# Kernel tuning notes

Measured on AMD Instinct MI355X. Metric: run time of the kernel, lower is better.

The kernel has to match this reference:

```python
import jax, jax.numpy as jnp
import numpy as np

DIM = 1024


def setup_inputs() -> dict:
    key = jax.random.key(0)
    ks = jax.random.split(key, 10)
    d = DIM
    return {
        "x": jax.random.normal(ks[0], (8, 4096, d), dtype=jnp.float32),
        "A": jax.random.normal(ks[1], (d, d), dtype=jnp.float32) * 0.1,
        "B": jax.random.normal(ks[2], (d, d), dtype=jnp.float32) * 0.1,
        "W_in": jax.random.normal(ks[3], (d, d), dtype=jnp.float32) * (1.0 / np.sqrt(d)),
        "b_in": jax.random.normal(ks[4], (d,), dtype=jnp.float32) * 0.01,
        "W_gate": jax.random.normal(ks[5], (d, d), dtype=jnp.float32) * (1.0 / np.sqrt(d)),
        "b_gate": jax.random.normal(ks[6], (d,), dtype=jnp.float32) * 0.01,
        "W_out": jax.random.normal(ks[7], (d, d), dtype=jnp.float32) * (1.0 / np.sqrt(d)),
        "b_out": jax.random.normal(ks[8], (d,), dtype=jnp.float32) * 0.01,
    }


def reference(x, A, B, W_in, b_in, W_gate, b_gate, W_out, b_out):
    # x: (batch, seq, dim)
    batch, seq, dim = x.shape
    # Timestep-independent projections hoisted out of the recurrence (same math).
    inp = jnp.einsum("bsd,ed->bse", x, W_in) + b_in          # in_proj(x[:, t]) for all t
    gate = jax.nn.sigmoid(jnp.einsum("bsd,ed->bse", inp, W_gate) + b_gate)
    u = jnp.einsum("bsd,ed->bse", inp, B)                     # inp @ B.T

    # Scan over time: state depends nonlinearly on previous state via A.
    def step(state, t):
        inp_t, gate_t, u_t = t                                 # each (batch, dim)
        s = jnp.tanh(state @ A.T + u_t)
        s = gate_t * s + (1.0 - gate_t) * inp_t
        return s, s

    init = jnp.zeros((batch, dim), dtype=x.dtype)
    xs = (
        jnp.swapaxes(inp, 0, 1),   # (seq, batch, dim)
        jnp.swapaxes(gate, 0, 1),
        jnp.swapaxes(u, 0, 1),
    )
    _, states = jax.lax.scan(step, init, xs)                   # (seq, batch, dim)
    out = jnp.einsum("sbd,ed->sbe", states, W_out) + b_out     # out_proj
    return jnp.swapaxes(out, 0, 1)                             # (batch, seq, dim)
```

## Files before the change

kernel.cpp:

```cpp
#include <hip/hip_runtime.h>
#include <stdint.h>


#define D 1024
#define NBATCH 8
#define SEQ 4096
#define NROWS 32768

static constexpr size_t GATE_BYTES  = (size_t)NROWS * D * 2;
static constexpr size_t U_BYTES     = (size_t)NROWS * D * 2;
static constexpr size_t SLICE_BYTES = (size_t)SEQ * NBATCH * D * 4;

typedef float f32x2 __attribute__((ext_vector_type(2)));
typedef float f32x4 __attribute__((ext_vector_type(4)));
typedef short bf16x8 __attribute__((ext_vector_type(8)));
typedef unsigned short u16x4 __attribute__((ext_vector_type(4)));
typedef unsigned short u16x8 __attribute__((ext_vector_type(8)));

#define MFMA16(a, b, c) __builtin_amdgcn_mfma_f32_16x16x32_bf16((a), (b), (c), 0, 0, 0)

__device__ __forceinline__ float bf2f(uint16_t h) {
  uint32_t u = ((uint32_t)h) << 16;
  return __builtin_bit_cast(float, u);
}
__device__ __forceinline__ uint16_t f2bf(float f) {
  uint32_t u = __builtin_bit_cast(uint32_t, f);
  u = u + 0x7fffu + ((u >> 16) & 1u);
  return (uint16_t)(u >> 16);
}
__device__ __forceinline__ void split1(float x, uint16_t& h, uint16_t& l) {
  const uint32_t xb = __builtin_bit_cast(uint32_t, x);
  h = (uint16_t)(xb >> 16);
  const float hr = __builtin_bit_cast(float, xb & 0xffff0000u);
  l = f2bf(x - hr);
}
__device__ __forceinline__ void split4(const float4 v, u16x4& h, u16x4& l) {
  uint16_t h0, l0, h1, l1, h2, l2, h3, l3;
  split1(v.x, h0, l0); split1(v.y, h1, l1);
  split1(v.z, h2, l2); split1(v.w, h3, l3);
  h = u16x4{h0, h1, h2, h3};
  l = u16x4{l0, l1, l2, l3};
}
__device__ __forceinline__ float fast_tanh(float x) {
  const float e = __expf(2.0f * x);
  return 1.0f - 2.0f / (e + 1.0f);
}

__global__ __launch_bounds__(256) void k_cvt(
    const float* __restrict__ S, uint16_t* __restrict__ H, uint16_t* __restrict__ L) {
  const int i = (blockIdx.x * 256 + threadIdx.x) << 2;
  const float4 v = *(const float4*)&S[i];
  u16x4 h, l;
  split4(v, h, l);
  *(u16x4*)&H[i] = h;
  *(u16x4*)&L[i] = l;
}


__global__ __launch_bounds__(256) void k_gemm_in(
    const float* __restrict__ X, const uint16_t* __restrict__ WhG,
    const uint16_t* __restrict__ WlG, const float* __restrict__ bias,
    uint16_t* __restrict__ Yh, uint16_t* __restrict__ Yl) {
  __shared__ uint16_t XhS[128][40], XlS[128][40];
  __shared__ uint16_t BhS[64][40], BlS[64][40];
  const int tid = threadIdx.x;
  const int w = tid >> 6, l = tid & 63;
  const int n0 = blockIdx.x << 6, m0 = blockIdx.y << 7;
  const int wr = w >> 1, wc = w & 1;
  f32x4 acc[4][2];
#pragma unroll
  for (int mt = 0; mt < 4; ++mt)
#pragma unroll
    for (int nt = 0; nt < 2; ++nt) acc[mt][nt] = f32x4{0.f, 0.f, 0.f, 0.f};

  const int xr = tid >> 3, xc = (tid & 7) << 2;
  const int br = tid >> 2, bc = (tid & 3) << 3;

  for (int k0 = 0; k0 < D; k0 += 32) {
    float4 xv[4];
#pragma unroll
    for (int q = 0; q < 4; ++q)
      xv[q] = *(const float4*)&X[(size_t)(m0 + xr + (q << 5)) * D + k0 + xc];
    const u16x8 wh = *(const u16x8*)&WhG[(size_t)(n0 + br) * D + k0 + bc];
    const u16x8 wl = *(const u16x8*)&WlG[(size_t)(n0 + br) * D + k0 + bc];
    __syncthreads();
#pragma unroll
    for (int q = 0; q < 4; ++q) {
      u16x4 h, lo;
      split4(xv[q], h, lo);
      *(u16x4*)&XhS[xr + (q << 5)][xc] = h;
      *(u16x4*)&XlS[xr + (q << 5)][xc] = lo;
    }
    *(u16x8*)&BhS[br][bc] = wh;
    *(u16x8*)&BlS[br][bc] = wl;
    __syncthreads();

    bf16x8 ah[4], al[4], bh[2], bl[2];
#pragma unroll
    for (int mt = 0; mt < 4; ++mt) {
      const int r = (wr << 6) + (mt << 4) + (l & 15), s = (l >> 4) << 3;
      ah[mt] = *(const bf16x8*)&XhS[r][s];
      al[mt] = *(const bf16x8*)&XlS[r][s];
    }
#pragma unroll
    for (int nt = 0; nt < 2; ++nt) {
      const int r = (wc << 5) + (nt << 4) + (l & 15), s = (l >> 4) << 3;
      bh[nt] = *(const bf16x8*)&BhS[r][s];
      bl[nt] = *(const bf16x8*)&BlS[r][s];
    }
#pragma unroll
    for (int mt = 0; mt < 4; ++mt)
#pragma unroll
      for (int nt = 0; nt < 2; ++nt) {
        acc[mt][nt] = MFMA16(ah[mt], bh[nt], acc[mt][nt]);
        acc[mt][nt] = MFMA16(ah[mt], bl[nt], acc[mt][nt]);
        acc[mt][nt] = MFMA16(al[mt], bh[nt], acc[mt][nt]);
      }
  }
#pragma unroll
  for (int mt = 0; mt < 4; ++mt)
#pragma unroll
    for (int nt = 0; nt < 2; ++nt) {
      const int col = n0 + (wc << 5) + (nt << 4) + (l & 15);
      const float bv = bias[col];
#pragma unroll
      for (int i = 0; i < 4; ++i) {
        const int row = m0 + (wr << 6) + (mt << 4) + ((l >> 4) << 2) + i;
        uint16_t hh, ll;
        split1(acc[mt][nt][i] + bv, hh, ll);
        Yh[(size_t)row * D + col] = hh;
        Yl[(size_t)row * D + col] = ll;
      }
    }
}

__global__ __launch_bounds__(256) void k_gemm_gate_u(
    const uint16_t* __restrict__ Ah, const uint16_t* __restrict__ Al,
    const uint16_t* __restrict__ WgH, const uint16_t* __restrict__ WgL,
    const uint16_t* __restrict__ BuH, const uint16_t* __restrict__ BuL,
    const float* __restrict__ bg,
    uint16_t* __restrict__ G, uint16_t* __restrict__ U) {
  __shared__ uint16_t XhS[128][40], XlS[128][40];
  __shared__ uint16_t GhS[64][40], GlS[64][40];
  __shared__ uint16_t UhS[64][40], UlS[64][40];
  const int tid = threadIdx.x;
  const int w = tid >> 6, l = tid & 63;
  const int n0 = blockIdx.x << 6, m0 = blockIdx.y << 7;
  const int wr = w >> 1, wc = w & 1;
  f32x4 accg[4][2], accu[4][2];
#pragma unroll
  for (int mt = 0; mt < 4; ++mt)
#pragma unroll
    for (int nt = 0; nt < 2; ++nt) {
      accg[mt][nt] = f32x4{0.f, 0.f, 0.f, 0.f};
      accu[mt][nt] = f32x4{0.f, 0.f, 0.f, 0.f};
    }
  const int ar = tid >> 2, ac = (tid & 3) << 3;

  for (int k0 = 0; k0 < D; k0 += 32) {
    u16x8 xh[2], xl[2];
#pragma unroll
    for (int q = 0; q < 2; ++q) {
      xh[q] = *(const u16x8*)&Ah[(size_t)(m0 + ar + (q << 6)) * D + k0 + ac];
      xl[q] = *(const u16x8*)&Al[(size_t)(m0 + ar + (q << 6)) * D + k0 + ac];
    }
    const u16x8 gh = *(const u16x8*)&WgH[(size_t)(n0 + ar) * D + k0 + ac];
    const u16x8 gl = *(const u16x8*)&WgL[(size_t)(n0 + ar) * D + k0 + ac];
    const u16x8 uh = *(const u16x8*)&BuH[(size_t)(n0 + ar) * D + k0 + ac];
    const u16x8 ul = *(const u16x8*)&BuL[(size_t)(n0 + ar) * D + k0 + ac];
    __syncthreads();
#pragma unroll
    for (int q = 0; q < 2; ++q) {
      *(u16x8*)&XhS[ar + (q << 6)][ac] = xh[q];
      *(u16x8*)&XlS[ar + (q << 6)][ac] = xl[q];
    }
    *(u16x8*)&GhS[ar][ac] = gh;
    *(u16x8*)&GlS[ar][ac] = gl;
    *(u16x8*)&UhS[ar][ac] = uh;
    *(u16x8*)&UlS[ar][ac] = ul;
    __syncthreads();

    bf16x8 ah[4], al[4];
#pragma unroll
    for (int mt = 0; mt < 4; ++mt) {
      const int r = (wr << 6) + (mt << 4) + (l & 15), s = (l >> 4) << 3;
      ah[mt] = *(const bf16x8*)&XhS[r][s];
      al[mt] = *(const bf16x8*)&XlS[r][s];
    }
#pragma unroll
    for (int nt = 0; nt < 2; ++nt) {
      const int r = (wc << 5) + (nt << 4) + (l & 15), s = (l >> 4) << 3;
      const bf16x8 bgh = *(const bf16x8*)&GhS[r][s];
      const bf16x8 bgl = *(const bf16x8*)&GlS[r][s];
      const bf16x8 buh = *(const bf16x8*)&UhS[r][s];
      const bf16x8 bul = *(const bf16x8*)&UlS[r][s];
#pragma unroll
      for (int mt = 0; mt < 4; ++mt) {
        accg[mt][nt] = MFMA16(ah[mt], bgh, accg[mt][nt]);
        accg[mt][nt] = MFMA16(ah[mt], bgl, accg[mt][nt]);
        accg[mt][nt] = MFMA16(al[mt], bgh, accg[mt][nt]);
        accu[mt][nt] = MFMA16(ah[mt], buh, accu[mt][nt]);
        accu[mt][nt] = MFMA16(ah[mt], bul, accu[mt][nt]);
        accu[mt][nt] = MFMA16(al[mt], buh, accu[mt][nt]);
      }
    }
  }
#pragma unroll
  for (int mt = 0; mt < 4; ++mt)
#pragma unroll
    for (int nt = 0; nt < 2; ++nt) {
      const int col = n0 + (wc << 5) + (nt << 4) + (l & 15);
      const float bv = bg[col];
#pragma unroll
      for (int i = 0; i < 4; ++i) {
        const int row = m0 + (wr << 6) + (mt << 4) + ((l >> 4) << 2) + i;
        const float z = accg[mt][nt][i] + bv;
        G[(size_t)row * D + col] = f2bf(1.0f / (1.0f + __expf(-z)));
        U[(size_t)row * D + col] = f2bf(accu[mt][nt][i]);
      }
    }
}

__global__ __launch_bounds__(256) void k_gemm_out(
    const float* __restrict__ S, const uint16_t* __restrict__ WhG,
    const uint16_t* __restrict__ WlG, const float* __restrict__ bias,
    float* __restrict__ Y) {
  __shared__ uint16_t XhS[128][40], XlS[128][40];
  __shared__ uint16_t BhS[64][40], BlS[64][40];
  const int tid = threadIdx.x;
  const int w = tid >> 6, l = tid & 63;
  const int n0 = blockIdx.x << 6, m0 = blockIdx.y << 7;
  const int wr = w >> 1, wc = w & 1;
  const int bb_ = m0 >> 12;
  f32x4 acc[4][2];
#pragma unroll
  for (int mt = 0; mt < 4; ++mt)
#pragma unroll
    for (int nt = 0; nt < 2; ++nt) acc[mt][nt] = f32x4{0.f, 0.f, 0.f, 0.f};

  const int xr = tid >> 3, xc = (tid & 7) << 2;
  const int br = tid >> 2, bc = (tid & 3) << 3;

  for (int k0 = 0; k0 < D; k0 += 32) {
    float4 xv[4];
#pragma unroll
    for (int q = 0; q < 4; ++q) {
      const int trow = (m0 & 4095) + xr + (q << 5);
      xv[q] = *(const float4*)&S[(((size_t)trow * NBATCH + bb_) << 10) + k0 + xc];
    }
    const u16x8 wh = *(const u16x8*)&WhG[(size_t)(n0 + br) * D + k0 + bc];
    const u16x8 wl = *(const u16x8*)&WlG[(size_t)(n0 + br) * D + k0 + bc];
    __syncthreads();
#pragma unroll
    for (int q = 0; q < 4; ++q) {
      u16x4 h, lo;
      split4(xv[q], h, lo);
      *(u16x4*)&XhS[xr + (q << 5)][xc] = h;
      *(u16x4*)&XlS[xr + (q << 5)][xc] = lo;
    }
    *(u16x8*)&BhS[br][bc] = wh;
    *(u16x8*)&BlS[br][bc] = wl;
    __syncthreads();

    bf16x8 ah[4], al[4], bh[2], bl[2];
#pragma unroll
    for (int mt = 0; mt < 4; ++mt) {
      const int r = (wr << 6) + (mt << 4) + (l & 15), s = (l >> 4) << 3;
      ah[mt] = *(const bf16x8*)&XhS[r][s];
      al[mt] = *(const bf16x8*)&XlS[r][s];
    }
#pragma unroll
    for (int nt = 0; nt < 2; ++nt) {
      const int r = (wc << 5) + (nt << 4) + (l & 15), s = (l >> 4) << 3;
      bh[nt] = *(const bf16x8*)&BhS[r][s];
      bl[nt] = *(const bf16x8*)&BlS[r][s];
    }
#pragma unroll
    for (int mt = 0; mt < 4; ++mt)
#pragma unroll
      for (int nt = 0; nt < 2; ++nt) {
        acc[mt][nt] = MFMA16(ah[mt], bh[nt], acc[mt][nt]);
        acc[mt][nt] = MFMA16(ah[mt], bl[nt], acc[mt][nt]);
        acc[mt][nt] = MFMA16(al[mt], bh[nt], acc[mt][nt]);
      }
  }
#pragma unroll
  for (int mt = 0; mt < 4; ++mt)
#pragma unroll
    for (int nt = 0; nt < 2; ++nt) {
      const int col = n0 + (wc << 5) + (nt << 4) + (l & 15);
      const float bv = bias[col];
#pragma unroll
      for (int i = 0; i < 4; ++i) {
        const int row = m0 + (wr << 6) + (mt << 4) + ((l >> 4) << 2) + i;
        Y[(size_t)row * D + col] = acc[mt][nt][i] + bv;
      }
    }
}

__device__ __forceinline__ int pidx(int g) { return g + (g >> 4); }

__global__ __launch_bounds__(256, 1)
__attribute__((amdgpu_waves_per_eu(1, 1)))
void k_scan(
    const float* __restrict__ A,
    const uint16_t* __restrict__ inph, const uint16_t* __restrict__ inpl,
    const uint16_t* __restrict__ gate, const uint16_t* __restrict__ u,
    float* __restrict__ slice) {
  __shared__ f32x2 Ss[2][544];
  const int tid = threadIdx.x;
  const int w = tid >> 6, l = tid & 63;
  const int b = blockIdx.x & 7;
  const int widx = blockIdx.x >> 3;
  const int j0 = (widx << 5) + (w << 3);

  f32x2 Areg[8][8];
#pragma unroll
  for (int c = 0; c < 8; ++c)
#pragma unroll
    for (int k = 0; k < 8; ++k) {
      const float2 t2 = *(const float2*)&A[(size_t)(j0 + c) * D + (k << 7) + (l << 1)];
      Areg[c][k] = f32x2{t2.x, t2.y};
    }
#pragma unroll
  for (int c = 0; c < 8; ++c)
#pragma unroll
    for (int k = 0; k < 8; ++k)
      asm volatile("" : "+v"(Areg[c][k].x), "+v"(Areg[c][k].y));

  unsigned long long* slice8 = (unsigned long long*)slice;
  const int jc = j0 + l;
  const int g0 = (w << 7) + l;
  const int pg0 = pidx(g0), pg1 = pidx(g0 + 64);

  for (int t = 0; t < SEQ; ++t) {
    float pg = 0.f, pu = 0.f, pi = 0.f;
    if (l < 8) {
      const size_t ridx = ((size_t)(b << 12) + t) * D + jc;
      pg = bf2f(gate[ridx]);
      pu = bf2f(u[ridx]);
      pi = bf2f(inph[ridx]) + bf2f(inpl[ridx]);
    }
    asm volatile("" : "+v"(pg), "+v"(pu), "+v"(pi));

    float f = 0.f;
    if (t > 0) {
      const unsigned long long* src8 =
          slice8 + (((size_t)(t - 1) * NBATCH + b) << 9);
      const uint32_t tagv = (uint32_t)(((t - 1) & 7) | 8);
      unsigned long long v0, v1;
      while (true) {
        v0 = __hip_atomic_load(&src8[g0],      __ATOMIC_RELAXED, __HIP_MEMORY_SCOPE_AGENT);
        v1 = __hip_atomic_load(&src8[g0 + 64], __ATOMIC_RELAXED, __HIP_MEMORY_SCOPE_AGENT);
        const bool ok = (((uint32_t)v0 & 15u) == tagv) & (((uint32_t)v1 & 15u) == tagv);
        if (__all(ok)) break;
        __builtin_amdgcn_s_sleep(1);
      }
      f32x2* buf = Ss[t & 1];
      buf[pg0] = __builtin_bit_cast(f32x2, v0);
      buf[pg1] = __builtin_bit_cast(f32x2, v1);
      __syncthreads();

      f32x2 acc[8];
#pragma unroll
      for (int c = 0; c < 8; ++c) acc[c] = f32x2{0.f, 0.f};
#pragma unroll
      for (int k = 0; k < 8; ++k) {
        const f32x2 sv = buf[pidx((k << 6) + l)];
#pragma unroll
        for (int c = 0; c < 8; ++c) acc[c] += sv * Areg[c][k];
      }
      float p[8];
#pragma unroll
      for (int c = 0; c < 8; ++c) p[c] = acc[c].x + acc[c].y;

      const bool b0 = (l & 1) != 0, b1 = (l & 2) != 0, b2 = (l & 4) != 0;
      float r[4];
#pragma unroll
      for (int i = 0; i < 4; ++i) {
        const float keep = b0 ? p[2 * i + 1] : p[2 * i];
        const float send = b0 ? p[2 * i] : p[2 * i + 1];
        r[i] = keep + __shfl_xor(send, 1, 64);
      }
      float q[2];
#pragma unroll
      for (int m = 0; m < 2; ++m) {
        const float keep = b1 ? r[2 * m + 1] : r[2 * m];
        const float send = b1 ? r[2 * m] : r[2 * m + 1];
        q[m] = keep + __shfl_xor(send, 2, 64);
      }
      {
        const float keep = b2 ? q[1] : q[0];
        const float send = b2 ? q[0] : q[1];
        f = keep + __shfl_xor(send, 4, 64);
      }
      f += __shfl_xor(f, 8, 64);
      f += __shfl_xor(f, 16, 64);
      f += __shfl_xor(f, 32, 64);
    }

    const float sv = fast_tanh(f + pu);
    const float val = pg * sv + (1.f - pg) * pi;

    const float valn = __shfl_xor(val, 1, 64);
    if ((l < 8) && ((l & 1) == 0)) {
      const uint32_t tagst = (uint32_t)((t & 7) | 8);
      const uint32_t lo = (__builtin_bit_cast(uint32_t, val) & ~15u) | tagst;
      const uint32_t hi = __builtin_bit_cast(uint32_t, valn);
      const unsigned long long pk = ((unsigned long long)hi << 32) | lo;
      __hip_atomic_store(&slice8[(((size_t)t * NBATCH + b) << 9) + ((j0 + l) >> 1)],
                         pk, __ATOMIC_RELAXED, __HIP_MEMORY_SCOPE_AGENT);
    }
  }
}

extern "C" void kernel_launch(void* const* d_in, const int* in_sizes, int n_in,
                              void* d_out, int out_size, void* d_ws, size_t ws_size,
                              hipStream_t stream) {
  const float* x      = (const float*)d_in[0];
  const float* A      = (const float*)d_in[1];
  const float* B      = (const float*)d_in[2];
  const float* W_in   = (const float*)d_in[3];
  const float* b_in   = (const float*)d_in[4];
  const float* W_gate = (const float*)d_in[5];
  const float* b_gate = (const float*)d_in[6];
  const float* W_out  = (const float*)d_in[7];
  const float* b_out  = (const float*)d_in[8];
  float* out = (float*)d_out;
  char* ws = (char*)d_ws;

  uint16_t* gateB = (uint16_t*)ws;
  uint16_t* uB    = (uint16_t*)(ws + GATE_BYTES);
  float* slice    = (float*)(ws + GATE_BYTES + U_BYTES);

  uint16_t* inph = (uint16_t*)d_out;
  uint16_t* inpl = inph + (size_t)NROWS * D;

  uint16_t* wslab = (uint16_t*)slice;
  uint16_t* winh = wslab + 0 * 1048576;
  uint16_t* winl = wslab + 1 * 1048576;
  uint16_t* wgh  = wslab + 2 * 1048576;
  uint16_t* wgl  = wslab + 3 * 1048576;
  uint16_t* buh  = wslab + 4 * 1048576;
  uint16_t* bul  = wslab + 5 * 1048576;
  uint16_t* woh  = (uint16_t*)ws;
  uint16_t* wol  = (uint16_t*)ws + 1048576;

  dim3 gg(D / 64, NROWS / 128);
  k_cvt<<<1024, 256, 0, stream>>>(W_in, winh, winl);
  k_cvt<<<1024, 256, 0, stream>>>(W_gate, wgh, wgl);
  k_cvt<<<1024, 256, 0, stream>>>(B, buh, bul);
  k_gemm_in<<<gg, 256, 0, stream>>>(x, winh, winl, b_in, inph, inpl);
  k_gemm_gate_u<<<gg, 256, 0, stream>>>(inph, inpl, wgh, wgl, buh, bul, b_gate, gateB, uB);
  hipMemsetAsync(slice, 0, SLICE_BYTES, stream);
  k_scan<<<256, 256, 0, stream>>>(A, inph, inpl, gateB, uB, slice);
  k_cvt<<<1024, 256, 0, stream>>>(W_out, woh, wol);
  k_gemm_out<<<gg, 256, 0, stream>>>(slice, woh, wol, b_out, out);
}
```

Measured before the change: 7.319 ms.

## Split scan workgroup into producer waves polling state and consumer compute waves

The scan kernel now launches 512 threads per block. Four extra producer waves poll the global state slice for each timestep's tagged values and copy them into a double-buffered LDS area. They signal the four compute waves through workgroup-scope rdy/done counters instead of a __syncthreads barrier. The goal is to hide the cross-block polling latency behind the matrix-vector work and cut barrier overhead. It adds spin-waiting on LDS counters, drops s_sleep, and relaxes the one-wave-per-EU occupancy constraint, so register pressure from Areg and the busy-wait contention could hurt.

```diff
diff --git a/kernel.cpp b/kernel.cpp
--- a/kernel.cpp
+++ b/kernel.cpp
@@ -300,20 +300,49 @@
 
 __device__ __forceinline__ int pidx(int g) { return g + (g >> 4); }
 
-__global__ __launch_bounds__(256, 1)
-__attribute__((amdgpu_waves_per_eu(1, 1)))
-void k_scan(
+__global__ __launch_bounds__(512, 2) void k_scan(
     const float* __restrict__ A,
     const uint16_t* __restrict__ inph, const uint16_t* __restrict__ inpl,
     const uint16_t* __restrict__ gate, const uint16_t* __restrict__ u,
     float* __restrict__ slice) {
   __shared__ f32x2 Ss[2][544];
+  __shared__ int rdy;
+  __shared__ int done;
   const int tid = threadIdx.x;
   const int w = tid >> 6, l = tid & 63;
   const int b = blockIdx.x & 7;
   const int widx = blockIdx.x >> 3;
+
+  if (tid == 0) { rdy = 0; done = 0; }
+  __syncthreads();
+
+  unsigned long long* slice8 = (unsigned long long*)slice;
+
+  if (w >= 4) {
+    const int q = w - 4;
+    const int g0 = (q << 7) + l;
+    const int pg0 = pidx(g0), pg1 = pidx(g0 + 64);
+    for (int ts = 0; ts < SEQ - 1; ++ts) {
+      const unsigned long long* src8 = slice8 + (((size_t)ts * NBATCH + b) << 9);
+      const uint32_t tagv = (uint32_t)((ts & 7) | 8);
+      unsigned long long v0, v1;
+      while (true) {
+        v0 = __hip_atomic_load(&src8[g0],      __ATOMIC_RELAXED, __HIP_MEMORY_SCOPE_AGENT);
+        v1 = __hip_atomic_load(&src8[g0 + 64], __ATOMIC_RELAXED, __HIP_MEMORY_SCOPE_AGENT);
+        const bool ok = (((uint32_t)v0 & 15u) == tagv) & (((uint32_t)v1 & 15u) == tagv);
+        if (__all(ok)) break;
+      }
+      while (__hip_atomic_load(&done, __ATOMIC_ACQUIRE, __HIP_MEMORY_SCOPE_WORKGROUP) < 4 * ts) {}
+      f32x2* buf = Ss[ts & 1];
+      buf[pg0] = __builtin_bit_cast(f32x2, v0);
+      buf[pg1] = __builtin_bit_cast(f32x2, v1);
+      if (l == 0)
+        __hip_atomic_fetch_add(&rdy, 1, __ATOMIC_RELEASE, __HIP_MEMORY_SCOPE_WORKGROUP);
+    }
+    return;
+  }
+
   const int j0 = (widx << 5) + (w << 3);
-
   f32x2 Areg[8][8];
 #pragma unroll
   for (int c = 0; c < 8; ++c)
@@ -328,10 +357,7 @@
     for (int k = 0; k < 8; ++k)
       asm volatile("" : "+v"(Areg[c][k].x), "+v"(Areg[c][k].y));
 
-  unsigned long long* slice8 = (unsigned long long*)slice;
   const int jc = j0 + l;
-  const int g0 = (w << 7) + l;
-  const int pg0 = pidx(g0), pg1 = pidx(g0 + 64);
 
   for (int t = 0; t < SEQ; ++t) {
     float pg = 0.f, pu = 0.f, pi = 0.f;
@@ -345,22 +371,8 @@
 
     float f = 0.f;
     if (t > 0) {
-      const unsigned long long* src8 =
-          slice8 + (((size_t)(t - 1) * NBATCH + b) << 9);
-      const uint32_t tagv = (uint32_t)(((t - 1) & 7) | 8);
-      unsigned long long v0, v1;
-      while (true) {
-        v0 = __hip_atomic_load(&src8[g0],      __ATOMIC_RELAXED, __HIP_MEMORY_SCOPE_AGENT);
-        v1 = __hip_atomic_load(&src8[g0 + 64], __ATOMIC_RELAXED, __HIP_MEMORY_SCOPE_AGENT);
-        const bool ok = (((uint32_t)v0 & 15u) == tagv) & (((uint32_t)v1 & 15u) == tagv);
-        if (__all(ok)) break;
-        __builtin_amdgcn_s_sleep(1);
-      }
-      f32x2* buf = Ss[t & 1];
-      buf[pg0] = __builtin_bit_cast(f32x2, v0);
-      buf[pg1] = __builtin_bit_cast(f32x2, v1);
-      __syncthreads();
-
+      while (__hip_atomic_load(&rdy, __ATOMIC_ACQUIRE, __HIP_MEMORY_SCOPE_WORKGROUP) < 4 * t) {}
+      const f32x2* buf = Ss[(t - 1) & 1];
       f32x2 acc[8];
 #pragma unroll
       for (int c = 0; c < 8; ++c) acc[c] = f32x2{0.f, 0.f};
@@ -370,6 +382,8 @@
 #pragma unroll
         for (int c = 0; c < 8; ++c) acc[c] += sv * Areg[c][k];
       }
+      if (l == 0)
+        __hip_atomic_fetch_add(&done, 1, __ATOMIC_RELEASE, __HIP_MEMORY_SCOPE_WORKGROUP);
       float p[8];
 #pragma unroll
       for (int c = 0; c < 8; ++c) p[c] = acc[c].x + acc[c].y;
@@ -382,21 +396,24 @@
         const float send = b0 ? p[2 * i] : p[2 * i + 1];
         r[i] = keep + __shfl_xor(send, 1, 64);
       }
-      float q[2];
+      float qv[2];
 #pragma unroll
       for (int m = 0; m < 2; ++m) {
         const float keep = b1 ? r[2 * m + 1] : r[2 * m];
         const float send = b1 ? r[2 * m] : r[2 * m + 1];
-        q[m] = keep + __shfl_xor(send, 2, 64);
+        qv[m] = keep + __shfl_xor(send, 2, 64);
       }
       {
-        const float keep = b2 ? q[1] : q[0];
-        const float send = b2 ? q[0] : q[1];
+        const float keep = b2 ? qv[1] : qv[0];
+        const float send = b2 ? qv[0] : qv[1];
         f = keep + __shfl_xor(send, 4, 64);
       }
       f += __shfl_xor(f, 8, 64);
       f += __shfl_xor(f, 16, 64);
       f += __shfl_xor(f, 32, 64);
+    } else {
+      if (l == 0)
+        __hip_atomic_fetch_add(&done, 1, __ATOMIC_RELEASE, __HIP_MEMORY_SCOPE_WORKGROUP);
     }
 
     const float sv = fast_tanh(f + pu);
@@ -453,7 +470,7 @@
   k_gemm_in<<<gg, 256, 0, stream>>>(x, winh, winl, b_in, inph, inpl);
   k_gemm_gate_u<<<gg, 256, 0, stream>>>(inph, inpl, wgh, wgl, buh, bul, b_gate, gateB, uB);
   hipMemsetAsync(slice, 0, SLICE_BYTES, stream);
-  k_scan<<<256, 256, 0, stream>>>(A, inph, inpl, gateB, uB, slice);
+  k_scan<<<256, 512, 0, stream>>>(A, inph, inpl, gateB, uB, slice);
   k_cvt<<<1024, 256, 0, stream>>>(W_out, woh, wol);
   k_gemm_out<<<gg, 256, 0, stream>>>(slice, woh, wol, b_out, out);
 }
```

Result: slower. 11.12 ms (+51.9%).
